# Performance work log

Hardware: AMD Instinct MI355X
Metric: run time of the kernel (lower is better)

## Reference

```python
import jax, jax.numpy as jnp
import numpy as np

S, B, D, H, DK, DFF, L, P = 128, 16, 512, 8, 64, 2048, 4, 4096


def setup_inputs() -> dict:
    key = jax.random.key(0)
    ks = jax.random.split(key, 10)
    def rn(k, shape, scale=0.02):
        return jax.random.normal(k, shape, jnp.float32) * scale
    return dict(
        x_seq=jax.random.normal(ks[0], (S, B, D), jnp.float32),
        w_query=rn(ks[1], (L, D, H * DK)),
        query_pos_bias=rn(ks[2], (L, H, DK)),
        key_pos_emb=rn(ks[3], (L, P, H, DK)),
        w_out=rn(ks[4], (L, D, D)), b_out=jnp.zeros((L, D), jnp.float32),
        ln1_g=jnp.ones((L, D), jnp.float32), ln1_b=jnp.zeros((L, D), jnp.float32),
        ln2_g=jnp.ones((L, D), jnp.float32), ln2_b=jnp.zeros((L, D), jnp.float32),
        w_ff1=rn(ks[5], (L, D, DFF)), b_ff1=jnp.zeros((L, DFF), jnp.float32),
        w_ff2=rn(ks[6], (L, DFF, D)), b_ff2=jnp.zeros((L, D), jnp.float32),
        norm_g=jnp.ones((D,), jnp.float32), norm_b=jnp.zeros((D,), jnp.float32),
        comb_w=jnp.ones((L + 1,), jnp.float32),
        w_key=rn(ks[7], (D, H * DK)), w_value=rn(ks[8], (D, H * DK)),
    )


def _layer_norm(x, g, b, eps=1e-5):
    mu = jnp.mean(x, -1, keepdims=True)
    var = jnp.mean((x - mu) ** 2, -1, keepdims=True)
    return (x - mu) * jax.lax.rsqrt(var + eps) * g + b


def reference(x_seq, w_query, query_pos_bias, key_pos_emb, w_out, b_out,
              ln1_g, ln1_b, ln2_g, ln2_b, w_ff1, b_ff1, w_ff2, b_ff2,
              norm_g, norm_b, comb_w, w_key, w_value):
    scale = 1.0 / jnp.sqrt(jnp.float32(DK))
    comb = jax.nn.softmax(comb_w)           # softmax over n_layers+1 weights
    jpos = jnp.arange(S)

    def step(carry, inp):
        mem_k, mem_v = carry                # [S, B, H, DK] growing KV memory stack
        x, t = inp                          # x: [B, D], t: scalar step index
        # valid memory slots are steps 0..t-1 (at t==0 attention is gated off below)
        valid = (jpos < jnp.maximum(t, 1))[:, None, None]   # [S,1,1]
        outs = [x]
        for l in range(L):
            # --- FeedbackAttention (pre-LN, relative key position embeddings) ---
            z = _layer_norm(x, ln1_g[l], ln1_b[l])
            q = (z @ w_query[l]).reshape(B, H, DK)
            # original: key_pos_embeddings[-t:]  ->  table index P - t + j for slot j
            kpe = jnp.take(key_pos_emb[l], jnp.clip(P - t + jpos, 0, P - 1), axis=0)  # [S,H,DK]
            ac = jnp.einsum('bhd,jbhd->jbh', q + query_pos_bias[l], mem_k)
            bd = jnp.einsum('bhd,jhd->jbh', q, kpe)
            scores = jnp.where(valid, (ac + bd) * scale, -1e9)
            attn = jax.nn.softmax(scores, axis=0)             # softmax over memory dim
            av = jnp.einsum('jbh,jbhd->bhd', attn, mem_v).reshape(B, D)
            x = jnp.where(t > 0, x + av @ w_out[l] + b_out[l], x)
            # --- FeedForward (pre-LN, ReLU) ---
            z = _layer_norm(x, ln2_g[l], ln2_b[l])
            x = x + jax.nn.relu(z @ w_ff1[l] + b_ff1[l]) @ w_ff2[l] + b_ff2[l]
            outs.append(x)
        # softmax-weighted combination of [input + layer outputs]
        mem = jnp.einsum('lbd,l->bd', jnp.stack(outs), comb)
        mem_k = mem_k.at[t].set((mem @ w_key).reshape(B, H, DK))
        mem_v = mem_v.at[t].set((mem @ w_value).reshape(B, H, DK))
        return (mem_k, mem_v), x

    mem0 = jnp.zeros((S, B, H, DK), x_seq.dtype)
    _, res = jax.lax.scan(jax.checkpoint(step), (mem0, mem0), (x_seq, jnp.arange(S)))
    return _layer_norm(res, norm_g, norm_b)
```

## Files before the change

kernel.cpp:

```cpp
#include <hip/hip_runtime.h>


#define S_ 128
#define B_ 16
#define D_ 512
#define H_ 8
#define DK_ 64
#define DFF_ 2048
#define L_ 4
#define P_ 4096

#define NBLK 128
#define NTHR 1024

struct FtkvParams {
  const float *x_seq, *w_query, *qpb, *kpe, *w_out, *b_out;
  const float *ln1_g, *ln1_b, *ln2_g, *ln2_b;
  const float *w_ff1, *b_ff1, *w_ff2, *b_ff2;
  const float *norm_g, *norm_b, *comb_w, *w_key, *w_value;
  float *out;
  float *dpart;
  float *dpart2;
  unsigned *memK;
  unsigned *memV;
  const uint4 *wqp;
  const uint4 *wop;
  const uint4 *w1p;
  const uint4 *w2p;
  const uint4 *wkp;
  const uint4 *wvp;
  unsigned int *bar;
};

__device__ __forceinline__ float cload(const float *p_) {
  return __hip_atomic_load(p_, __ATOMIC_RELAXED, __HIP_MEMORY_SCOPE_AGENT);
}
__device__ __forceinline__ void cstore(float *p_, float v) {
  __hip_atomic_store(p_, v, __ATOMIC_RELAXED, __HIP_MEMORY_SCOPE_AGENT);
}

__device__ __forceinline__ float waveRedSum(float v) {
#pragma unroll
  for (int off = 32; off; off >>= 1) v += __shfl_xor(v, off, 64);
  return v;
}
__device__ __forceinline__ float waveRedMax(float v) {
#pragma unroll
  for (int off = 32; off; off >>= 1) v = fmaxf(v, __shfl_xor(v, off, 64));
  return v;
}

__device__ __forceinline__ void lbar() {
  asm volatile("s_waitcnt lgkmcnt(0)" ::: "memory");
  __builtin_amdgcn_s_barrier();
}

#define UNPK(w, flo, fhi)                                     \
  float flo = __uint_as_float((unsigned)(w) << 16);           \
  float fhi = __uint_as_float((unsigned)(w) & 0xffff0000u);

__device__ __forceinline__ float dot8(const float *z, uint4 w) {
  UNPK(w.x, a0, a1); UNPK(w.y, b0, b1);
  UNPK(w.z, c0, c1); UNPK(w.w, d0, d1);
  return ((z[0] * a0 + z[1] * a1) + (z[2] * b0 + z[3] * b1)) +
         ((z[4] * c0 + z[5] * c1) + (z[6] * d0 + z[7] * d1));
}

__device__ __forceinline__ void gbarN(unsigned *arr, unsigned &epoch) {
  __syncthreads();
  const unsigned e = ++epoch;
  if (threadIdx.x == 0) {
    __hip_atomic_fetch_add(arr, 1u, __ATOMIC_RELAXED,
                           __HIP_MEMORY_SCOPE_AGENT);
    while (__hip_atomic_load(arr, __ATOMIC_RELAXED,
                             __HIP_MEMORY_SCOPE_AGENT) < e * 8u)
      __builtin_amdgcn_s_sleep(1);
  }
  __syncthreads();
}

__global__ void ftkv_init(unsigned *bar) {
  for (int i = threadIdx.x; i < 4096; i += 256) bar[i] = 0u;
}

__device__ __forceinline__ unsigned bf16rne(float x) {
  unsigned b = __float_as_uint(x);
  return (b + 0x7fffu + ((b >> 16) & 1u)) >> 16;
}

__global__ void ftkv_pack(const float *src, unsigned *dst, int K, int N) {
  int total = (K / 2) * N;
  int n4 = N * 4;
  for (int i = blockIdx.x * blockDim.x + threadIdx.x; i < total;
       i += gridDim.x * blockDim.x) {
    int k8 = i / n4, rem = i - k8 * n4;
    int col = rem >> 2, q = rem & 3;
    int r0 = 8 * k8 + 2 * q;
    dst[i] = bf16rne(src[(size_t)r0 * N + col]) |
             (bf16rne(src[(size_t)(r0 + 1) * N + col]) << 16);
  }
}

struct Smem {
  float sZ[512];
  float sP[1024];
  float sH[256];
  float sQ[64], sQB[64], sS[128], sRed[24];
};

__device__ __forceinline__ void lnstats(int tid, int lane, int wid, float v,
                                        float *sRed, float &mu, float &rs) {
  lbar();
  if (tid < 512) {
    float s1 = waveRedSum(v), s2 = waveRedSum(v * v);
    if (lane == 0) { sRed[wid] = s1; sRed[8 + wid] = s2; }
  }
  lbar();
  float a = 0.f, c = 0.f;
#pragma unroll
  for (int i = 0; i < 8; ++i) { a += sRed[i]; c += sRed[8 + i]; }
  mu = a * (1.f / 512.f);
  float var = c * (1.f / 512.f) - mu * mu;
  rs = rsqrtf(var + 1e-5f);
}

__global__ __launch_bounds__(NTHR, 4) void ftkv_main(FtkvParams p) {
  const int bid = blockIdx.x;
  const int tid = threadIdx.x;
  const int lane = tid & 63, wid = tid >> 6;
  const int g = bid >> 3;
  const int cs = bid & 7;

  __shared__ Smem sm;

  unsigned *garr = p.bar + g * 32;
  unsigned gep = 0;

  float cw0 = p.comb_w[0], cw1 = p.comb_w[1], cw2 = p.comb_w[2],
        cw3 = p.comb_w[3], cw4 = p.comb_w[4];
  float cm = fmaxf(fmaxf(fmaxf(cw0, cw1), fmaxf(cw2, cw3)), cw4);
  float e0 = __expf(cw0 - cm), e1 = __expf(cw1 - cm), e2 = __expf(cw2 - cm),
        e3 = __expf(cw3 - cm), e4 = __expf(cw4 - cm);
  float einv = 1.0f / (e0 + e1 + e2 + e3 + e4);
  float comb0 = e0 * einv, comb1 = e1 * einv, comb2 = e2 * einv,
        comb3 = e3 * einv, comb4 = e4 * einv;

  float xr = 0.f, mr = 0.f;
  if (tid < 512) {
    xr = p.x_seq[g * D_ + tid];
    mr = comb0 * xr;
  }

  unsigned *memKb = p.memK + ((size_t)(g * H_ + cs)) * S_ * 32;
  unsigned *memVb = p.memV + ((size_t)(g * H_ + cs)) * S_ * 32;

  const int d6 = tid & 63, ks16 = tid >> 6;
  const int j7 = tid & 127, ds8 = tid >> 7;
  const int col9 = tid & 511, ks2 = tid >> 9;
  const int c8 = tid & 255, ksb = tid >> 8;

  for (int t = 0; t < S_; ++t) {
    for (int l = 0; l < L_; ++l) {
      const float cl = (l == 1) ? comb1 : (l == 2) ? comb2 : comb3;

      if (l > 0 && tid < 512) {
        float s = p.b_ff2[(l - 1) * D_ + tid];
#pragma unroll
        for (int c2 = 0; c2 < 8; ++c2)
          s += cload(&p.dpart2[((size_t)g * 8 + c2) * D_ + tid]);
        xr += s;
        mr += cl * xr;
      }

      if (t > 0) {
        uint4 wq[4], wo[4];
        {
          const uint4 *wqp = p.wqp + (size_t)l * 64 * 512 + cs * 64 + d6;
#pragma unroll
          for (int j = 0; j < 4; ++j) wq[j] = wqp[(size_t)(ks16 * 4 + j) * 512];
          const uint4 *wop = p.wop + (size_t)l * 64 * 512 + col9;
#pragma unroll
          for (int j = 0; j < 4; ++j)
            wo[j] = wop[(size_t)(cs * 8 + ks2 * 4 + j) * 512];
        }
        uint4 mku = ((const uint4 *)(memKb + (size_t)j7 * 32))[ds8];
        int kidx = P_ - t + j7;
        kidx = kidx < 0 ? 0 : (kidx > P_ - 1 ? P_ - 1 : kidx);
        const float4 *kpp = (const float4 *)(p.kpe +
            (((size_t)l * P_ + kidx) * H_ + cs) * 64 + ds8 * 8);
        float4 kp0 = kpp[0], kp1 = kpp[1];
        unsigned mvp[8];
        {
#pragma unroll
          for (int jj = 0; jj < 8; ++jj)
            mvp[jj] = memVb[(size_t)(ks16 * 8 + jj) * 32 + (d6 >> 1)];
        }

        float mu, rs;
        lnstats(tid, lane, wid, xr, sm.sRed, mu, rs);
        if (tid < 512)
          sm.sZ[tid] = (xr - mu) * rs * p.ln1_g[l * D_ + tid] +
                       p.ln1_b[l * D_ + tid];
        lbar();
        {
          float acc = 0.f;
#pragma unroll
          for (int j = 0; j < 4; ++j)
            acc += dot8(&sm.sZ[8 * (ks16 * 4 + j)], wq[j]);
          sm.sP[tid] = acc;
        }
        lbar();
        if (tid < 64) {
          float q = 0.f;
#pragma unroll
          for (int ks = 0; ks < 16; ++ks) q += sm.sP[ks * 64 + tid];
          sm.sQ[tid] = q;
          sm.sQB[tid] = q + p.qpb[(l * H_ + cs) * 64 + tid];
        }
        lbar();
        {
          UNPK(mku.x, k0, k1); UNPK(mku.y, k2, k3);
          UNPK(mku.z, k4, k5); UNPK(mku.w, k6, k7);
          const float *qb = &sm.sQB[ds8 * 8], *qr = &sm.sQ[ds8 * 8];
          float acc =
              (qb[0] * k0 + qb[1] * k1 + qb[2] * k2 + qb[3] * k3) +
              (qb[4] * k4 + qb[5] * k5 + qb[6] * k6 + qb[7] * k7) +
              (qr[0] * kp0.x + qr[1] * kp0.y + qr[2] * kp0.z + qr[3] * kp0.w) +
              (qr[4] * kp1.x + qr[5] * kp1.y + qr[6] * kp1.z + qr[7] * kp1.w);
          sm.sP[tid] = acc;
        }
        lbar();
        if (tid < 128) {
          float sc = ((sm.sP[tid] + sm.sP[tid + 128]) +
                      (sm.sP[tid + 256] + sm.sP[tid + 384])) +
                     ((sm.sP[tid + 512] + sm.sP[tid + 640]) +
                      (sm.sP[tid + 768] + sm.sP[tid + 896]));
          sm.sS[tid] = (tid < t) ? sc * 0.125f : -1e30f;
        }
        lbar();
        if (tid < 64) {
          float a0 = sm.sS[tid], a1 = sm.sS[tid + 64];
          float m = waveRedMax(fmaxf(a0, a1));
          float ee0 = __expf(a0 - m), ee1 = __expf(a1 - m);
          float s = waveRedSum(ee0 + ee1);
          sm.sS[tid] = ee0;
          sm.sS[64 + tid] = ee1;
          if (tid == 0) sm.sRed[19] = s;
        }
        lbar();
        {
          float acc = 0.f;
#pragma unroll
          for (int jj = 0; jj < 8; ++jj) {
            UNPK(mvp[jj], v0, v1);
            float vv = (d6 & 1) ? v1 : v0;
            acc += sm.sS[ks16 * 8 + jj] * vv;
          }
          sm.sP[tid] = acc;
        }
        lbar();
        if (tid < 64) {
          float a = 0.f;
#pragma unroll
          for (int js = 0; js < 16; ++js) a += sm.sP[js * 64 + tid];
          sm.sQ[tid] = a / sm.sRed[19];
        }
        lbar();
        {
          float acc = 0.f;
#pragma unroll
          for (int j = 0; j < 4; ++j)
            acc += dot8(&sm.sQ[8 * (ks2 * 4 + j)], wo[j]);
          sm.sP[tid] = acc;
        }
        lbar();
        if (tid < 512)
          cstore(&p.dpart[((size_t)g * 8 + cs) * D_ + tid],
                 sm.sP[tid] + sm.sP[512 + tid]);
        gbarN(garr, gep);

        if (tid < 512) {
          float s = p.b_out[l * D_ + tid];
#pragma unroll
          for (int c2 = 0; c2 < 8; ++c2)
            s += cload(&p.dpart[((size_t)g * 8 + c2) * D_ + tid]);
          xr += s;
        }
      }

      {
        uint4 w1r[16];
        {
          const uint4 *w1 = p.w1p + (size_t)l * 64 * DFF_ + cs * 256 + c8;
#pragma unroll
          for (int j = 0; j < 16; ++j)
            w1r[j] = w1[(size_t)(ksb * 16 + j) * DFF_];
        }
        float mu, rs;
        lnstats(tid, lane, wid, xr, sm.sRed, mu, rs);
        if (tid < 512)
          sm.sZ[tid] = (xr - mu) * rs * p.ln2_g[l * D_ + tid] +
                       p.ln2_b[l * D_ + tid];
        lbar();
        {
          float acc = 0.f;
#pragma unroll
          for (int j = 0; j < 16; ++j)
            acc += dot8(&sm.sZ[8 * (ksb * 16 + j)], w1r[j]);
          sm.sP[tid] = acc;
        }
        uint4 w2r[16];
        {
          const uint4 *w2 = p.w2p + (size_t)l * 256 * 512 + col9;
#pragma unroll
          for (int j = 0; j < 16; ++j)
            w2r[j] = w2[(size_t)(cs * 32 + ks2 * 16 + j) * 512];
        }
        lbar();
        if (tid < 256) {
          float h = ((sm.sP[tid] + sm.sP[256 + tid]) +
                     (sm.sP[512 + tid] + sm.sP[768 + tid])) +
                    p.b_ff1[l * DFF_ + cs * 256 + tid];
          sm.sH[tid] = fmaxf(h, 0.f);
        }
        lbar();
        {
          float acc = 0.f;
#pragma unroll
          for (int j = 0; j < 16; ++j)
            acc += dot8(&sm.sH[8 * (ks2 * 16 + j)], w2r[j]);
          sm.sP[tid] = acc;
        }
        lbar();
        if (tid < 512)
          cstore(&p.dpart2[((size_t)g * 8 + cs) * D_ + tid],
                 sm.sP[tid] + sm.sP[512 + tid]);
      }
      gbarN(garr, gep);
    }

    {
      const int kv = tid >> 9, rE = tid & 511, dE = rE & 63, ks8 = rE >> 6;
      uint4 wkv[8];
      {
        const uint4 *w4 = (kv ? p.wvp : p.wkp) + cs * 64 + dE;
#pragma unroll
        for (int j = 0; j < 8; ++j) wkv[j] = w4[(size_t)(ks8 * 8 + j) * 512];
      }
      if (tid < 512) {
        float s = p.b_ff2[3 * D_ + tid];
#pragma unroll
        for (int c2 = 0; c2 < 8; ++c2)
          s += cload(&p.dpart2[((size_t)g * 8 + c2) * D_ + tid]);
        xr += s;
        mr += comb4 * xr;
        sm.sZ[tid] = mr;
      }
      lbar();
      {
        float acc = 0.f;
#pragma unroll
        for (int j = 0; j < 8; ++j)
          acc += dot8(&sm.sZ[8 * (ks8 * 8 + j)], wkv[j]);
        sm.sP[tid] = acc;
      }
      lbar();
      if (tid < 128) {
        int kv2 = tid >> 6, d = tid & 63;
        float v = 0.f;
#pragma unroll
        for (int ks = 0; ks < 8; ++ks) v += sm.sP[kv2 * 512 + ks * 64 + d];
        sm.sS[tid] = v;
      }
      lbar();
      if (tid < 64) {
        int kv2 = tid >> 5, d2 = tid & 31;
        float lo = sm.sS[kv2 * 64 + 2 * d2], hi = sm.sS[kv2 * 64 + 2 * d2 + 1];
        unsigned pk = bf16rne(lo) | (bf16rne(hi) << 16);
        unsigned *dst = kv2 ? memVb : memKb;
        dst[(size_t)t * 32 + d2] = pk;
      }
      __syncthreads();
      float mu, rs;
      lnstats(tid, lane, wid, xr, sm.sRed, mu, rs);
      if (tid < 512 && (tid >> 6) == cs)
        p.out[((size_t)t * B_ + g) * D_ + tid] =
            (xr - mu) * rs * p.norm_g[tid] + p.norm_b[tid];
      if (t + 1 < S_ && tid < 512) {
        xr = p.x_seq[((size_t)(t + 1) * B_ + g) * D_ + tid];
        mr = comb0 * xr;
      }
    }
  }
}

extern "C" void kernel_launch(void *const *d_in, const int *in_sizes, int n_in,
                              void *d_out, int out_size, void *d_ws,
                              size_t ws_size, hipStream_t stream) {
  (void)in_sizes; (void)n_in; (void)out_size; (void)ws_size;

  FtkvParams p;
  p.x_seq  = (const float *)d_in[0];
  p.w_query = (const float *)d_in[1];
  p.qpb    = (const float *)d_in[2];
  p.kpe    = (const float *)d_in[3];
  p.w_out  = (const float *)d_in[4];
  p.b_out  = (const float *)d_in[5];
  p.ln1_g  = (const float *)d_in[6];
  p.ln1_b  = (const float *)d_in[7];
  p.ln2_g  = (const float *)d_in[8];
  p.ln2_b  = (const float *)d_in[9];
  p.w_ff1  = (const float *)d_in[10];
  p.b_ff1  = (const float *)d_in[11];
  p.w_ff2  = (const float *)d_in[12];
  p.b_ff2  = (const float *)d_in[13];
  p.norm_g = (const float *)d_in[14];
  p.norm_b = (const float *)d_in[15];
  p.comb_w = (const float *)d_in[16];
  p.w_key  = (const float *)d_in[17];
  p.w_value = (const float *)d_in[18];
  p.out = (float *)d_out;

  char *ws = (char *)d_ws;
  p.bar = (unsigned int *)ws;
  float *f = (float *)(ws + 16384);
  p.dpart  = f; f += B_ * 8 * D_;
  p.dpart2 = f; f += B_ * 8 * D_;
  unsigned *u = (unsigned *)f;
  p.memK = u; u += B_ * H_ * S_ * 32;
  p.memV = u; u += B_ * H_ * S_ * 32;
  unsigned *wqp = u; u += L_ * 256 * 512;
  unsigned *wop = u; u += L_ * 256 * 512;
  unsigned *w1p = u; u += L_ * 256 * DFF_;
  unsigned *w2p = u; u += L_ * 1024 * 512;
  unsigned *wkp = u; u += 256 * 512;
  unsigned *wvp = u; u += 256 * 512;
  p.wqp = (const uint4 *)wqp; p.wop = (const uint4 *)wop;
  p.w1p = (const uint4 *)w1p; p.w2p = (const uint4 *)w2p;
  p.wkp = (const uint4 *)wkp; p.wvp = (const uint4 *)wvp;

  ftkv_init<<<dim3(1), dim3(256), 0, stream>>>(p.bar);
  for (int l = 0; l < L_; ++l) {
    ftkv_pack<<<dim3(256), dim3(256), 0, stream>>>(
        p.w_query + (size_t)l * 512 * 512, wqp + (size_t)l * 256 * 512, 512, 512);
    ftkv_pack<<<dim3(256), dim3(256), 0, stream>>>(
        p.w_out + (size_t)l * 512 * 512, wop + (size_t)l * 256 * 512, 512, 512);
    ftkv_pack<<<dim3(512), dim3(256), 0, stream>>>(
        p.w_ff1 + (size_t)l * 512 * DFF_, w1p + (size_t)l * 256 * DFF_, 512, DFF_);
    ftkv_pack<<<dim3(512), dim3(256), 0, stream>>>(
        p.w_ff2 + (size_t)l * DFF_ * 512, w2p + (size_t)l * 1024 * 512, DFF_, 512);
  }
  ftkv_pack<<<dim3(256), dim3(256), 0, stream>>>(p.w_key, wkp, 512, 512);
  ftkv_pack<<<dim3(256), dim3(256), 0, stream>>>(p.w_value, wvp, 512, 512);
  ftkv_main<<<dim3(NBLK), dim3(NTHR), 0, stream>>>(p);
}
```

Measured before the change: 11.66 ms.

## Prefetch next-layer attention operands across barriers and map blocks by XCC

Moves the loads of query weights, K/V memory and key position embeddings for the next layer/step before the group barrier, so their latency overlaps barrier waiting. Also assigns block roles at runtime from the hardware XCC ID so that blocks sharing a column slice of weights run on the same XCD, improving L2 reuse. Adds registers kept live across barriers and an atomic-based assignment protocol at startup.

```diff
diff --git a/kernel.cpp b/kernel.cpp
--- a/kernel.cpp
+++ b/kernel.cpp
@@ -38,6 +38,9 @@
 __device__ __forceinline__ void cstore(float *p_, float v) {
   __hip_atomic_store(p_, v, __ATOMIC_RELAXED, __HIP_MEMORY_SCOPE_AGENT);
 }
+__device__ __forceinline__ unsigned aload(const unsigned *p_) {
+  return __hip_atomic_load(p_, __ATOMIC_RELAXED, __HIP_MEMORY_SCOPE_AGENT);
+}
 
 __device__ __forceinline__ float waveRedSum(float v) {
 #pragma unroll
@@ -80,7 +83,7 @@
 }
 
 __global__ void ftkv_init(unsigned *bar) {
-  for (int i = threadIdx.x; i < 4096; i += 256) bar[i] = 0u;
+  for (int i = threadIdx.x; i < 5120; i += 256) bar[i] = 0u;
 }
 
 __device__ __forceinline__ unsigned bf16rne(float x) {
@@ -124,14 +127,65 @@
   rs = rsqrtf(var + 1e-5f);
 }
 
+#define ISSUE_A(lA, tA)                                                     \
+  do {                                                                      \
+    const uint4 *wqp_ = p.wqp + (size_t)(lA) * 64 * 512 + cs * 64 + d6;     \
+    _Pragma("unroll") for (int j_ = 0; j_ < 4; ++j_)                        \
+        wqN[j_] = wqp_[(size_t)(ks16 * 4 + j_) * 512];                      \
+    mkuN = ((const uint4 *)(memKb + (size_t)j7 * 32))[ds8];                 \
+    int kidx_ = P_ - (tA) + j7;                                             \
+    kidx_ = kidx_ < 0 ? 0 : (kidx_ > P_ - 1 ? P_ - 1 : kidx_);              \
+    const float4 *kpp_ = (const float4 *)(p.kpe +                           \
+        (((size_t)(lA) * P_ + kidx_) * H_ + cs) * 64 + ds8 * 8);            \
+    kpN0 = kpp_[0];                                                         \
+    kpN1 = kpp_[1];                                                         \
+    _Pragma("unroll") for (int jj_ = 0; jj_ < 8; ++jj_)                     \
+        mvpN[jj_] = memVb[(size_t)(ks16 * 8 + jj_) * 32 + (d6 >> 1)];       \
+  } while (0)
+
 __global__ __launch_bounds__(NTHR, 4) void ftkv_main(FtkvParams p) {
-  const int bid = blockIdx.x;
   const int tid = threadIdx.x;
   const int lane = tid & 63, wid = tid >> 6;
-  const int g = bid >> 3;
-  const int cs = bid & 7;
 
   __shared__ Smem sm;
+  __shared__ int sAssign[2];
+
+  if (tid == 0) {
+    unsigned x;
+    asm volatile("s_getreg_b32 %0, hwreg(HW_REG_XCC_ID)" : "=s"(x));
+    x &= 7u;
+    unsigned *cnt = p.bar + 2048;
+    unsigned *excess = p.bar + 2304;
+    unsigned n = __hip_atomic_fetch_add(&cnt[x * 32], 1u, __ATOMIC_RELAXED,
+                                        __HIP_MEMORY_SCOPE_AGENT);
+    int mycs, myg;
+    if (n < 16u) {
+      mycs = (int)x;
+      myg = (int)n;
+    } else {
+      for (;;) {
+        unsigned s = 0;
+        for (int i = 0; i < 8; ++i) s += aload(&cnt[i * 32]);
+        if (s >= (unsigned)NBLK) break;
+        __builtin_amdgcn_s_sleep(8);
+      }
+      unsigned e = __hip_atomic_fetch_add(excess, 1u, __ATOMIC_RELAXED,
+                                          __HIP_MEMORY_SCOPE_AGENT);
+      mycs = 0; myg = 0;
+      for (int c = 0; c < 8; ++c) {
+        unsigned cc = aload(&cnt[c * 32]);
+        unsigned used = cc < 16u ? cc : 16u;
+        unsigned fr = 16u - used;
+        if (e < fr) { mycs = c; myg = (int)(used + e); break; }
+        e -= fr;
+      }
+    }
+    sAssign[0] = myg;
+    sAssign[1] = mycs;
+  }
+  __syncthreads();
+  const int g = sAssign[0];
+  const int cs = sAssign[1];
 
   unsigned *garr = p.bar + g * 32;
   unsigned gep = 0;
@@ -153,12 +207,18 @@
 
   unsigned *memKb = p.memK + ((size_t)(g * H_ + cs)) * S_ * 32;
   unsigned *memVb = p.memV + ((size_t)(g * H_ + cs)) * S_ * 32;
+  float *dpA = p.dpart + (size_t)g * 8 * 512;
+  float *dpB = p.dpart2 + (size_t)g * 8 * 512;
 
   const int d6 = tid & 63, ks16 = tid >> 6;
   const int j7 = tid & 127, ds8 = tid >> 7;
   const int col9 = tid & 511, ks2 = tid >> 9;
   const int c8 = tid & 255, ksb = tid >> 8;
 
+  uint4 wqN[4], mkuN;
+  float4 kpN0, kpN1;
+  unsigned mvpN[8];
+
   for (int t = 0; t < S_; ++t) {
     for (int l = 0; l < L_; ++l) {
       const float cl = (l == 1) ? comb1 : (l == 2) ? comb2 : comb3;
@@ -166,34 +226,18 @@
       if (l > 0 && tid < 512) {
         float s = p.b_ff2[(l - 1) * D_ + tid];
 #pragma unroll
-        for (int c2 = 0; c2 < 8; ++c2)
-          s += cload(&p.dpart2[((size_t)g * 8 + c2) * D_ + tid]);
+        for (int c2 = 0; c2 < 8; ++c2) s += cload(dpB + c2 * 512 + tid);
         xr += s;
         mr += cl * xr;
       }
 
       if (t > 0) {
-        uint4 wq[4], wo[4];
-        {
-          const uint4 *wqp = p.wqp + (size_t)l * 64 * 512 + cs * 64 + d6;
-#pragma unroll
-          for (int j = 0; j < 4; ++j) wq[j] = wqp[(size_t)(ks16 * 4 + j) * 512];
+        uint4 wo[4];
+        {
           const uint4 *wop = p.wop + (size_t)l * 64 * 512 + col9;
 #pragma unroll
           for (int j = 0; j < 4; ++j)
             wo[j] = wop[(size_t)(cs * 8 + ks2 * 4 + j) * 512];
-        }
-        uint4 mku = ((const uint4 *)(memKb + (size_t)j7 * 32))[ds8];
-        int kidx = P_ - t + j7;
-        kidx = kidx < 0 ? 0 : (kidx > P_ - 1 ? P_ - 1 : kidx);
-        const float4 *kpp = (const float4 *)(p.kpe +
-            (((size_t)l * P_ + kidx) * H_ + cs) * 64 + ds8 * 8);
-        float4 kp0 = kpp[0], kp1 = kpp[1];
-        unsigned mvp[8];
-        {
-#pragma unroll
-          for (int jj = 0; jj < 8; ++jj)
-            mvp[jj] = memVb[(size_t)(ks16 * 8 + jj) * 32 + (d6 >> 1)];
         }
 
         float mu, rs;
@@ -206,7 +250,7 @@
           float acc = 0.f;
 #pragma unroll
           for (int j = 0; j < 4; ++j)
-            acc += dot8(&sm.sZ[8 * (ks16 * 4 + j)], wq[j]);
+            acc += dot8(&sm.sZ[8 * (ks16 * 4 + j)], wqN[j]);
           sm.sP[tid] = acc;
         }
         lbar();
@@ -219,14 +263,14 @@
         }
         lbar();
         {
-          UNPK(mku.x, k0, k1); UNPK(mku.y, k2, k3);
-          UNPK(mku.z, k4, k5); UNPK(mku.w, k6, k7);
+          UNPK(mkuN.x, k0, k1); UNPK(mkuN.y, k2, k3);
+          UNPK(mkuN.z, k4, k5); UNPK(mkuN.w, k6, k7);
           const float *qb = &sm.sQB[ds8 * 8], *qr = &sm.sQ[ds8 * 8];
           float acc =
               (qb[0] * k0 + qb[1] * k1 + qb[2] * k2 + qb[3] * k3) +
               (qb[4] * k4 + qb[5] * k5 + qb[6] * k6 + qb[7] * k7) +
-              (qr[0] * kp0.x + qr[1] * kp0.y + qr[2] * kp0.z + qr[3] * kp0.w) +
-              (qr[4] * kp1.x + qr[5] * kp1.y + qr[6] * kp1.z + qr[7] * kp1.w);
+              (qr[0] * kpN0.x + qr[1] * kpN0.y + qr[2] * kpN0.z + qr[3] * kpN0.w) +
+              (qr[4] * kpN1.x + qr[5] * kpN1.y + qr[6] * kpN1.z + qr[7] * kpN1.w);
           sm.sP[tid] = acc;
         }
         lbar();
@@ -252,7 +296,7 @@
           float acc = 0.f;
 #pragma unroll
           for (int jj = 0; jj < 8; ++jj) {
-            UNPK(mvp[jj], v0, v1);
+            UNPK(mvpN[jj], v0, v1);
             float vv = (d6 & 1) ? v1 : v0;
             acc += sm.sS[ks16 * 8 + jj] * vv;
           }
@@ -275,15 +319,13 @@
         }
         lbar();
         if (tid < 512)
-          cstore(&p.dpart[((size_t)g * 8 + cs) * D_ + tid],
-                 sm.sP[tid] + sm.sP[512 + tid]);
+          cstore(dpA + cs * 512 + tid, sm.sP[tid] + sm.sP[512 + tid]);
         gbarN(garr, gep);
 
         if (tid < 512) {
           float s = p.b_out[l * D_ + tid];
 #pragma unroll
-          for (int c2 = 0; c2 < 8; ++c2)
-            s += cload(&p.dpart[((size_t)g * 8 + c2) * D_ + tid]);
+          for (int c2 = 0; c2 < 8; ++c2) s += cload(dpA + c2 * 512 + tid);
           xr += s;
         }
       }
@@ -333,9 +375,9 @@
         }
         lbar();
         if (tid < 512)
-          cstore(&p.dpart2[((size_t)g * 8 + cs) * D_ + tid],
-                 sm.sP[tid] + sm.sP[512 + tid]);
-      }
+          cstore(dpB + cs * 512 + tid, sm.sP[tid] + sm.sP[512 + tid]);
+      }
+      if (t > 0 && l + 1 < L_) ISSUE_A(l + 1, t);
       gbarN(garr, gep);
     }
 
@@ -350,8 +392,7 @@
       if (tid < 512) {
         float s = p.b_ff2[3 * D_ + tid];
 #pragma unroll
-        for (int c2 = 0; c2 < 8; ++c2)
-          s += cload(&p.dpart2[((size_t)g * 8 + c2) * D_ + tid]);
+        for (int c2 = 0; c2 < 8; ++c2) s += cload(dpB + c2 * 512 + tid);
         xr += s;
         mr += comb4 * xr;
         sm.sZ[tid] = mr;
@@ -390,6 +431,7 @@
         xr = p.x_seq[((size_t)(t + 1) * B_ + g) * D_ + tid];
         mr = comb0 * xr;
       }
+      if (t + 1 < S_) ISSUE_A(0, t + 1);
     }
   }
 }
@@ -423,7 +465,7 @@
 
   char *ws = (char *)d_ws;
   p.bar = (unsigned int *)ws;
-  float *f = (float *)(ws + 16384);
+  float *f = (float *)(ws + 20480);
   p.dpart  = f; f += B_ * 8 * D_;
   p.dpart2 = f; f += B_ * 8 * D_;
   unsigned *u = (unsigned *)f;
```

Result: slower. 18.09 ms (+55.2%).

## Transpose packed weights to column-major and reduce matvecs with wave shuffles

Applied to the files above, without the earlier changes.

Repacks all bf16 weight matrices column-major (K contiguous per output column) and stores V memory transposed. Each wavefront now computes whole output columns and reduces with cross-lane shuffles instead of writing partial sums to shared memory and doing a separate reduction pass. This removes the large sP shared buffer and several block barriers per layer. The cost is that weights are no longer all prefetched into registers before LayerNorm; only the first tile is prefetched and the rest are loaded inside the compute loops, which may expose memory latency.

```diff
diff --git a/kernel.cpp b/kernel.cpp
--- a/kernel.cpp
+++ b/kernel.cpp
@@ -22,13 +22,13 @@
   float *dpart;
   float *dpart2;
   unsigned *memK;
-  unsigned *memV;
-  const uint4 *wqp;
-  const uint4 *wop;
-  const uint4 *w1p;
-  const uint4 *w2p;
-  const uint4 *wkp;
-  const uint4 *wvp;
+  ushort *memVT;
+  const uint4 *wqT;
+  const uint4 *woT;
+  const uint4 *w1T;
+  const uint4 *w2T;
+  const uint4 *wkT;
+  const uint4 *wvT;
   unsigned int *bar;
 };
 
@@ -47,6 +47,20 @@
 __device__ __forceinline__ float waveRedMax(float v) {
 #pragma unroll
   for (int off = 32; off; off >>= 1) v = fmaxf(v, __shfl_xor(v, off, 64));
+  return v;
+}
+__device__ __forceinline__ float red8(float v) {
+  v += __shfl_xor(v, 1, 64);
+  v += __shfl_xor(v, 2, 64);
+  v += __shfl_xor(v, 4, 64);
+  return v;
+}
+__device__ __forceinline__ float red32(float v) {
+  v += __shfl_xor(v, 1, 64);
+  v += __shfl_xor(v, 2, 64);
+  v += __shfl_xor(v, 4, 64);
+  v += __shfl_xor(v, 8, 64);
+  v += __shfl_xor(v, 16, 64);
   return v;
 }
 
@@ -88,22 +102,21 @@
   return (b + 0x7fffu + ((b >> 16) & 1u)) >> 16;
 }
 
-__global__ void ftkv_pack(const float *src, unsigned *dst, int K, int N) {
-  int total = (K / 2) * N;
-  int n4 = N * 4;
+__global__ void ftkv_packT(const float *src, unsigned *dst, int K, int N) {
+  int kd = K / 2;
+  int total = kd * N;
   for (int i = blockIdx.x * blockDim.x + threadIdx.x; i < total;
        i += gridDim.x * blockDim.x) {
-    int k8 = i / n4, rem = i - k8 * n4;
-    int col = rem >> 2, q = rem & 3;
+    int n = i / kd, rem = i - n * kd;
+    int k8 = rem >> 2, q = rem & 3;
     int r0 = 8 * k8 + 2 * q;
-    dst[i] = bf16rne(src[(size_t)r0 * N + col]) |
-             (bf16rne(src[(size_t)(r0 + 1) * N + col]) << 16);
+    dst[i] = bf16rne(src[(size_t)r0 * N + n]) |
+             (bf16rne(src[(size_t)(r0 + 1) * N + n]) << 16);
   }
 }
 
 struct Smem {
   float sZ[512];
-  float sP[1024];
   float sH[256];
   float sQ[64], sQB[64], sS[128], sRed[24];
 };
@@ -127,7 +140,7 @@
 __global__ __launch_bounds__(NTHR, 4) void ftkv_main(FtkvParams p) {
   const int bid = blockIdx.x;
   const int tid = threadIdx.x;
-  const int lane = tid & 63, wid = tid >> 6;
+  const int lane = tid & 63, wv = tid >> 6;
   const int g = bid >> 3;
   const int cs = bid & 7;
 
@@ -152,12 +165,9 @@
   }
 
   unsigned *memKb = p.memK + ((size_t)(g * H_ + cs)) * S_ * 32;
-  unsigned *memVb = p.memV + ((size_t)(g * H_ + cs)) * S_ * 32;
-
-  const int d6 = tid & 63, ks16 = tid >> 6;
-  const int j7 = tid & 127, ds8 = tid >> 7;
-  const int col9 = tid & 511, ks2 = tid >> 9;
-  const int c8 = tid & 255, ksb = tid >> 8;
+  ushort *memVTb = p.memVT + ((size_t)(g * H_ + cs)) * 64 * S_;
+  float *dpA = p.dpart + (size_t)g * 8 * 512;
+  float *dpB = p.dpart2 + (size_t)g * 8 * 512;
 
   for (int t = 0; t < S_; ++t) {
     for (int l = 0; l < L_; ++l) {
@@ -166,80 +176,75 @@
       if (l > 0 && tid < 512) {
         float s = p.b_ff2[(l - 1) * D_ + tid];
 #pragma unroll
-        for (int c2 = 0; c2 < 8; ++c2)
-          s += cload(&p.dpart2[((size_t)g * 8 + c2) * D_ + tid]);
+        for (int c2 = 0; c2 < 8; ++c2) s += cload(dpB + c2 * 512 + tid);
         xr += s;
         mr += cl * xr;
       }
 
       if (t > 0) {
-        uint4 wq[4], wo[4];
-        {
-          const uint4 *wqp = p.wqp + (size_t)l * 64 * 512 + cs * 64 + d6;
-#pragma unroll
-          for (int j = 0; j < 4; ++j) wq[j] = wqp[(size_t)(ks16 * 4 + j) * 512];
-          const uint4 *wop = p.wop + (size_t)l * 64 * 512 + col9;
-#pragma unroll
-          for (int j = 0; j < 4; ++j)
-            wo[j] = wop[(size_t)(cs * 8 + ks2 * 4 + j) * 512];
-        }
-        uint4 mku = ((const uint4 *)(memKb + (size_t)j7 * 32))[ds8];
-        int kidx = P_ - t + j7;
+        const uint4 *wqTl =
+            p.wqT + (size_t)l * 512 * 64 + (size_t)(cs * 64) * 64;
+        const uint4 *woTl =
+            p.woT + ((size_t)l * H_ + cs) * 512 * 8;
+
+        uint4 pfWq = wqTl[(size_t)(wv * 4) * 64 + lane];
+        const int jj = lane >> 3, u8 = lane & 7;
+        const int jsc = wv * 8 + jj;
+        uint4 pfMku = ((const uint4 *)(memKb + (size_t)jsc * 32))[u8];
+        int kidx = P_ - t + jsc;
         kidx = kidx < 0 ? 0 : (kidx > P_ - 1 ? P_ - 1 : kidx);
         const float4 *kpp = (const float4 *)(p.kpe +
-            (((size_t)l * P_ + kidx) * H_ + cs) * 64 + ds8 * 8);
-        float4 kp0 = kpp[0], kp1 = kpp[1];
-        unsigned mvp[8];
-        {
-#pragma unroll
-          for (int jj = 0; jj < 8; ++jj)
-            mvp[jj] = memVb[(size_t)(ks16 * 8 + jj) * 32 + (d6 >> 1)];
-        }
+            (((size_t)l * P_ + kidx) * H_ + cs) * 64 + u8 * 8);
+        float4 pfKp0 = kpp[0], pfKp1 = kpp[1];
+        unsigned pfMv =
+            *(const unsigned *)(memVTb + (size_t)(wv * 4) * S_ + 2 * lane);
+        uint4 pfWo = woTl[(size_t)(wv * 32 + jj) * 8 + u8];
 
         float mu, rs;
-        lnstats(tid, lane, wid, xr, sm.sRed, mu, rs);
+        lnstats(tid, lane, wv, xr, sm.sRed, mu, rs);
         if (tid < 512)
           sm.sZ[tid] = (xr - mu) * rs * p.ln1_g[l * D_ + tid] +
                        p.ln1_b[l * D_ + tid];
         lbar();
         {
-          float acc = 0.f;
-#pragma unroll
-          for (int j = 0; j < 4; ++j)
-            acc += dot8(&sm.sZ[8 * (ks16 * 4 + j)], wq[j]);
-          sm.sP[tid] = acc;
-        }
-        lbar();
-        if (tid < 64) {
-          float q = 0.f;
-#pragma unroll
-          for (int ks = 0; ks < 16; ++ks) q += sm.sP[ks * 64 + tid];
-          sm.sQ[tid] = q;
-          sm.sQB[tid] = q + p.qpb[(l * H_ + cs) * 64 + tid];
-        }
-        lbar();
-        {
-          UNPK(mku.x, k0, k1); UNPK(mku.y, k2, k3);
-          UNPK(mku.z, k4, k5); UNPK(mku.w, k6, k7);
-          const float *qb = &sm.sQB[ds8 * 8], *qr = &sm.sQ[ds8 * 8];
+          float qv[4];
+#pragma unroll
+          for (int c = 0; c < 4; ++c) {
+            int col = wv * 4 + c;
+            uint4 w = (c == 0) ? pfWq : wqTl[(size_t)col * 64 + lane];
+            qv[c] = dot8(&sm.sZ[8 * lane], w);
+          }
+#pragma unroll
+          for (int c = 0; c < 4; ++c) qv[c] = waveRedSum(qv[c]);
+          if (lane == 0) {
+#pragma unroll
+            for (int c = 0; c < 4; ++c) {
+              int col = wv * 4 + c;
+              sm.sQ[col] = qv[c];
+              sm.sQB[col] = qv[c] + p.qpb[(l * H_ + cs) * 64 + col];
+            }
+          }
+        }
+        lbar();
+        {
+          UNPK(pfMku.x, k0, k1); UNPK(pfMku.y, k2, k3);
+          UNPK(pfMku.z, k4, k5); UNPK(pfMku.w, k6, k7);
+          const float *qb = &sm.sQB[u8 * 8], *qr = &sm.sQ[u8 * 8];
           float acc =
               (qb[0] * k0 + qb[1] * k1 + qb[2] * k2 + qb[3] * k3) +
               (qb[4] * k4 + qb[5] * k5 + qb[6] * k6 + qb[7] * k7) +
-              (qr[0] * kp0.x + qr[1] * kp0.y + qr[2] * kp0.z + qr[3] * kp0.w) +
-              (qr[4] * kp1.x + qr[5] * kp1.y + qr[6] * kp1.z + qr[7] * kp1.w);
-          sm.sP[tid] = acc;
-        }
-        lbar();
-        if (tid < 128) {
-          float sc = ((sm.sP[tid] + sm.sP[tid + 128]) +
-                      (sm.sP[tid + 256] + sm.sP[tid + 384])) +
-                     ((sm.sP[tid + 512] + sm.sP[tid + 640]) +
-                      (sm.sP[tid + 768] + sm.sP[tid + 896]));
-          sm.sS[tid] = (tid < t) ? sc * 0.125f : -1e30f;
+              (qr[0] * pfKp0.x + qr[1] * pfKp0.y + qr[2] * pfKp0.z +
+               qr[3] * pfKp0.w) +
+              (qr[4] * pfKp1.x + qr[5] * pfKp1.y + qr[6] * pfKp1.z +
+               qr[7] * pfKp1.w);
+          acc = red8(acc);
+          if (u8 == 0) sm.sS[jsc] = acc;
         }
         lbar();
         if (tid < 64) {
           float a0 = sm.sS[tid], a1 = sm.sS[tid + 64];
+          a0 = (tid < t) ? a0 * 0.125f : -1e30f;
+          a1 = (tid + 64 < t) ? a1 * 0.125f : -1e30f;
           float m = waveRedMax(fmaxf(a0, a1));
           float ee0 = __expf(a0 - m), ee1 = __expf(a1 - m);
           float s = waveRedSum(ee0 + ee1);
@@ -249,140 +254,128 @@
         }
         lbar();
         {
-          float acc = 0.f;
-#pragma unroll
-          for (int jj = 0; jj < 8; ++jj) {
-            UNPK(mvp[jj], v0, v1);
-            float vv = (d6 & 1) ? v1 : v0;
-            acc += sm.sS[ks16 * 8 + jj] * vv;
-          }
-          sm.sP[tid] = acc;
-        }
-        lbar();
-        if (tid < 64) {
-          float a = 0.f;
-#pragma unroll
-          for (int js = 0; js < 16; ++js) a += sm.sP[js * 64 + tid];
-          sm.sQ[tid] = a / sm.sRed[19];
-        }
-        lbar();
-        {
-          float acc = 0.f;
-#pragma unroll
-          for (int j = 0; j < 4; ++j)
-            acc += dot8(&sm.sQ[8 * (ks2 * 4 + j)], wo[j]);
-          sm.sP[tid] = acc;
-        }
-        lbar();
-        if (tid < 512)
-          cstore(&p.dpart[((size_t)g * 8 + cs) * D_ + tid],
-                 sm.sP[tid] + sm.sP[512 + tid]);
+          float av4[4];
+#pragma unroll
+          for (int c = 0; c < 4; ++c) {
+            int d = wv * 4 + c;
+            unsigned mv = (c == 0)
+                ? pfMv
+                : *(const unsigned *)(memVTb + (size_t)d * S_ + 2 * lane);
+            UNPK(mv, v0, v1);
+            av4[c] = sm.sS[2 * lane] * v0 + sm.sS[2 * lane + 1] * v1;
+          }
+#pragma unroll
+          for (int c = 0; c < 4; ++c) av4[c] = waveRedSum(av4[c]);
+          if (lane == 0) {
+            float inv = 1.0f / sm.sRed[19];
+#pragma unroll
+            for (int c = 0; c < 4; ++c) sm.sQ[wv * 4 + c] = av4[c] * inv;
+          }
+        }
+        lbar();
+        {
+          float res[4];
+#pragma unroll
+          for (int pp = 0; pp < 4; ++pp) {
+            int col = wv * 32 + pp * 8 + jj;
+            uint4 w = (pp == 0) ? pfWo : woTl[(size_t)col * 8 + u8];
+            float part = dot8(&sm.sQ[8 * u8], w);
+            res[pp] = red8(part);
+          }
+#pragma unroll
+          for (int pp = 0; pp < 4; ++pp)
+            if (u8 == 0)
+              cstore(dpA + cs * 512 + wv * 32 + pp * 8 + jj, res[pp]);
+        }
         gbarN(garr, gep);
 
         if (tid < 512) {
           float s = p.b_out[l * D_ + tid];
 #pragma unroll
-          for (int c2 = 0; c2 < 8; ++c2)
-            s += cload(&p.dpart[((size_t)g * 8 + c2) * D_ + tid]);
+          for (int c2 = 0; c2 < 8; ++c2) s += cload(dpA + c2 * 512 + tid);
           xr += s;
         }
       }
 
       {
-        uint4 w1r[16];
-        {
-          const uint4 *w1 = p.w1p + (size_t)l * 64 * DFF_ + cs * 256 + c8;
-#pragma unroll
-          for (int j = 0; j < 16; ++j)
-            w1r[j] = w1[(size_t)(ksb * 16 + j) * DFF_];
-        }
+        const uint4 *w1Tl =
+            p.w1T + (size_t)l * 2048 * 64 + (size_t)(cs * 256) * 64;
+        const uint4 *w2Tl = p.w2T + (size_t)l * 512 * 256;
+        const int csub2 = lane >> 5, u32 = lane & 31;
+
+        uint4 pfW1 = w1Tl[(size_t)wv * 64 + lane];
+        uint4 pfW2 =
+            w2Tl[(size_t)(wv * 2 + csub2) * 256 + cs * 32 + u32];
+
         float mu, rs;
-        lnstats(tid, lane, wid, xr, sm.sRed, mu, rs);
+        lnstats(tid, lane, wv, xr, sm.sRed, mu, rs);
         if (tid < 512)
           sm.sZ[tid] = (xr - mu) * rs * p.ln2_g[l * D_ + tid] +
                        p.ln2_b[l * D_ + tid];
         lbar();
         {
-          float acc = 0.f;
-#pragma unroll
-          for (int j = 0; j < 16; ++j)
-            acc += dot8(&sm.sZ[8 * (ksb * 16 + j)], w1r[j]);
-          sm.sP[tid] = acc;
-        }
-        uint4 w2r[16];
-        {
-          const uint4 *w2 = p.w2p + (size_t)l * 256 * 512 + col9;
-#pragma unroll
-          for (int j = 0; j < 16; ++j)
-            w2r[j] = w2[(size_t)(cs * 32 + ks2 * 16 + j) * 512];
-        }
-        lbar();
-        if (tid < 256) {
-          float h = ((sm.sP[tid] + sm.sP[256 + tid]) +
-                     (sm.sP[512 + tid] + sm.sP[768 + tid])) +
-                    p.b_ff1[l * DFF_ + cs * 256 + tid];
-          sm.sH[tid] = fmaxf(h, 0.f);
-        }
-        lbar();
-        {
-          float acc = 0.f;
-#pragma unroll
-          for (int j = 0; j < 16; ++j)
-            acc += dot8(&sm.sH[8 * (ks2 * 16 + j)], w2r[j]);
-          sm.sP[tid] = acc;
-        }
-        lbar();
-        if (tid < 512)
-          cstore(&p.dpart2[((size_t)g * 8 + cs) * D_ + tid],
-                 sm.sP[tid] + sm.sP[512 + tid]);
+#pragma unroll
+          for (int pp = 0; pp < 16; ++pp) {
+            int col = pp * 16 + wv;
+            uint4 w = (pp == 0) ? pfW1 : w1Tl[(size_t)col * 64 + lane];
+            float part = dot8(&sm.sZ[8 * lane], w);
+            part = waveRedSum(part);
+            if (lane == 0)
+              sm.sH[col] =
+                  fmaxf(part + p.b_ff1[l * DFF_ + cs * 256 + col], 0.f);
+          }
+        }
+        lbar();
+        {
+#pragma unroll
+          for (int pp = 0; pp < 16; ++pp) {
+            int col = pp * 32 + wv * 2 + csub2;
+            uint4 w =
+                (pp == 0) ? pfW2 : w2Tl[(size_t)col * 256 + cs * 32 + u32];
+            float part = dot8(&sm.sH[8 * u32], w);
+            part = red32(part);
+            if (u32 == 0) cstore(dpB + cs * 512 + col, part);
+          }
+        }
       }
       gbarN(garr, gep);
     }
 
     {
-      const int kv = tid >> 9, rE = tid & 511, dE = rE & 63, ks8 = rE >> 6;
-      uint4 wkv[8];
-      {
-        const uint4 *w4 = (kv ? p.wvp : p.wkp) + cs * 64 + dE;
-#pragma unroll
-        for (int j = 0; j < 8; ++j) wkv[j] = w4[(size_t)(ks8 * 8 + j) * 512];
-      }
+      uint4 pfKv = p.wkT[(size_t)(cs * 64 + wv) * 64 + lane];
       if (tid < 512) {
         float s = p.b_ff2[3 * D_ + tid];
 #pragma unroll
-        for (int c2 = 0; c2 < 8; ++c2)
-          s += cload(&p.dpart2[((size_t)g * 8 + c2) * D_ + tid]);
+        for (int c2 = 0; c2 < 8; ++c2) s += cload(dpB + c2 * 512 + tid);
         xr += s;
         mr += comb4 * xr;
         sm.sZ[tid] = mr;
       }
       lbar();
       {
-        float acc = 0.f;
-#pragma unroll
-        for (int j = 0; j < 8; ++j)
-          acc += dot8(&sm.sZ[8 * (ks8 * 8 + j)], wkv[j]);
-        sm.sP[tid] = acc;
+#pragma unroll
+        for (int pp = 0; pp < 8; ++pp) {
+          int o = pp * 16 + wv;
+          int c = o & 63;
+          const uint4 *wt = (o < 64) ? p.wkT : p.wvT;
+          uint4 w = (pp == 0) ? pfKv : wt[(size_t)(cs * 64 + c) * 64 + lane];
+          float part = dot8(&sm.sZ[8 * lane], w);
+          part = waveRedSum(part);
+          if (lane == 0) sm.sS[o] = part;
+        }
       }
       lbar();
-      if (tid < 128) {
-        int kv2 = tid >> 6, d = tid & 63;
-        float v = 0.f;
-#pragma unroll
-        for (int ks = 0; ks < 8; ++ks) v += sm.sP[kv2 * 512 + ks * 64 + d];
-        sm.sS[tid] = v;
-      }
-      lbar();
-      if (tid < 64) {
-        int kv2 = tid >> 5, d2 = tid & 31;
-        float lo = sm.sS[kv2 * 64 + 2 * d2], hi = sm.sS[kv2 * 64 + 2 * d2 + 1];
-        unsigned pk = bf16rne(lo) | (bf16rne(hi) << 16);
-        unsigned *dst = kv2 ? memVb : memKb;
-        dst[(size_t)t * 32 + d2] = pk;
+      if (tid < 32) {
+        unsigned pk =
+            bf16rne(sm.sS[2 * tid]) | (bf16rne(sm.sS[2 * tid + 1]) << 16);
+        memKb[(size_t)t * 32 + tid] = pk;
+      } else if (tid >= 64 && tid < 128) {
+        int d = tid - 64;
+        memVTb[(size_t)d * S_ + t] = (ushort)bf16rne(sm.sS[64 + d]);
       }
       __syncthreads();
       float mu, rs;
-      lnstats(tid, lane, wid, xr, sm.sRed, mu, rs);
+      lnstats(tid, lane, wv, xr, sm.sRed, mu, rs);
       if (tid < 512 && (tid >> 6) == cs)
         p.out[((size_t)t * B_ + g) * D_ + tid] =
             (xr - mu) * rs * p.norm_g[tid] + p.norm_b[tid];
@@ -428,29 +421,34 @@
   p.dpart2 = f; f += B_ * 8 * D_;
   unsigned *u = (unsigned *)f;
   p.memK = u; u += B_ * H_ * S_ * 32;
-  p.memV = u; u += B_ * H_ * S_ * 32;
-  unsigned *wqp = u; u += L_ * 256 * 512;
-  unsigned *wop = u; u += L_ * 256 * 512;
-  unsigned *w1p = u; u += L_ * 256 * DFF_;
-  unsigned *w2p = u; u += L_ * 1024 * 512;
-  unsigned *wkp = u; u += 256 * 512;
-  unsigned *wvp = u; u += 256 * 512;
-  p.wqp = (const uint4 *)wqp; p.wop = (const uint4 *)wop;
-  p.w1p = (const uint4 *)w1p; p.w2p = (const uint4 *)w2p;
-  p.wkp = (const uint4 *)wkp; p.wvp = (const uint4 *)wvp;
+  p.memVT = (ushort *)u; u += B_ * H_ * 64 * S_ / 2;
+  unsigned *wqT = u; u += L_ * 512 * 256;
+  unsigned *woT = u; u += L_ * H_ * 512 * 32;
+  unsigned *w1T = u; u += L_ * 2048 * 256;
+  unsigned *w2T = u; u += (size_t)L_ * 512 * 1024;
+  unsigned *wkT = u; u += 512 * 256;
+  unsigned *wvT = u; u += 512 * 256;
+  p.wqT = (const uint4 *)wqT; p.woT = (const uint4 *)woT;
+  p.w1T = (const uint4 *)w1T; p.w2T = (const uint4 *)w2T;
+  p.wkT = (const uint4 *)wkT; p.wvT = (const uint4 *)wvT;
 
   ftkv_init<<<dim3(1), dim3(256), 0, stream>>>(p.bar);
   for (int l = 0; l < L_; ++l) {
-    ftkv_pack<<<dim3(256), dim3(256), 0, stream>>>(
-        p.w_query + (size_t)l * 512 * 512, wqp + (size_t)l * 256 * 512, 512, 512);
-    ftkv_pack<<<dim3(256), dim3(256), 0, stream>>>(
-        p.w_out + (size_t)l * 512 * 512, wop + (size_t)l * 256 * 512, 512, 512);
-    ftkv_pack<<<dim3(512), dim3(256), 0, stream>>>(
-        p.w_ff1 + (size_t)l * 512 * DFF_, w1p + (size_t)l * 256 * DFF_, 512, DFF_);
-    ftkv_pack<<<dim3(512), dim3(256), 0, stream>>>(
-        p.w_ff2 + (size_t)l * DFF_ * 512, w2p + (size_t)l * 1024 * 512, DFF_, 512);
-  }
-  ftkv_pack<<<dim3(256), dim3(256), 0, stream>>>(p.w_key, wkp, 512, 512);
-  ftkv_pack<<<dim3(256), dim3(256), 0, stream>>>(p.w_value, wvp, 512, 512);
+    ftkv_packT<<<dim3(512), dim3(256), 0, stream>>>(
+        p.w_query + (size_t)l * 512 * 512, wqT + (size_t)l * 512 * 256,
+        512, 512);
+    for (int h = 0; h < H_; ++h)
+      ftkv_packT<<<dim3(128), dim3(256), 0, stream>>>(
+          p.w_out + ((size_t)l * 512 + h * 64) * 512,
+          woT + ((size_t)l * H_ + h) * 512 * 32, 64, 512);
+    ftkv_packT<<<dim3(512), dim3(256), 0, stream>>>(
+        p.w_ff1 + (size_t)l * 512 * DFF_, w1T + (size_t)l * 2048 * 256,
+        512, DFF_);
+    ftkv_packT<<<dim3(512), dim3(256), 0, stream>>>(
+        p.w_ff2 + (size_t)l * DFF_ * 512, w2T + (size_t)l * 512 * 1024,
+        DFF_, 512);
+  }
+  ftkv_packT<<<dim3(512), dim3(256), 0, stream>>>(p.w_key, wkT, 512, 512);
+  ftkv_packT<<<dim3(512), dim3(256), 0, stream>>>(p.w_value, wvT, 512, 512);
   ftkv_main<<<dim3(NBLK), dim3(NTHR), 0, stream>>>(p);
 }
```

New measurement: 23.27 ms. 2x slower.
